# Optimization experiments

Hardware: AMD Instinct MI355X
Metric: run time of the kernel (lower is better)

Reference implementation:

```python
import jax, jax.numpy as jnp
import numpy as np

BATCH = 2048
NUM_SEEN = 32768
HIDDEN = 768
GAMMA_INIT = -2.3


def setup_inputs() -> dict:
    key = jax.random.key(0)
    k_h, k_s, k_v, k_g = jax.random.split(key, 4)
    h = jax.random.normal(k_h, (BATCH, HIDDEN), dtype=jnp.float32)
    # sigmoid gate scores in [0, 1]
    s = jax.random.uniform(k_s, (BATCH, NUM_SEEN), dtype=jnp.float32)
    # unit spurious directions (rows normalized, as in set_directions usage)
    V = jax.random.normal(k_v, (NUM_SEEN, HIDDEN), dtype=jnp.float32)
    V = V / jnp.linalg.norm(V, axis=1, keepdims=True)
    log_gamma = jnp.float32(GAMMA_INIT)
    return {"h": h, "s": s, "V": V, "log_gamma": log_gamma, "top_k": 64}


def top_k_gate(s, k):
    # keep top-k scores per row, zero the rest
    if k <= 0:
        return s
    k = min(k, s.shape[1])
    vals, idx = jax.lax.top_k(s, k)            # [B, k]
    rows = jnp.arange(s.shape[0])[:, None]      # [B, 1]
    return jnp.zeros_like(s).at[rows, idx].set(vals)


def reference(h, s, V, log_gamma, top_k):
    gamma = jax.nn.softplus(log_gamma)
    s_sparse = top_k_gate(s, top_k)
    proj = h @ V.T                              # [B, num_seen]
    raw_signal = (s_sparse * proj) @ V          # [B, hidden]
    return h - gamma * raw_signal
```

## Files before the change

kernel.cpp:

```cpp
#include <hip/hip_runtime.h>
#include <math.h>


constexpr int NSEEN  = 32768;
constexpr int HIDDEN = 768;
constexpr int NBINS  = 2048;
constexpr int SEG    = NBINS / 256;
constexpr int CAP    = 2048;
constexpr int KMAX   = 64;

__device__ inline unsigned int ordkey(float x) {
    unsigned int u = __float_as_uint(x);
    return (u & 0x80000000u) ? ~u : (u | 0x80000000u);
}
__device__ inline float ordkey_inv(unsigned int o) {
    unsigned int u = (o & 0x80000000u) ? (o ^ 0x80000000u) : ~o;
    return __uint_as_float(u);
}

__device__ inline int bucket_of(float x, int mode, float lo, float scale) {
    if (mode == 0) {
        if (x < lo) return -1;
        int b = (int)((x - lo) * scale);
        return (b > NBINS - 1) ? (NBINS - 1) : b;
    } else {
        return (int)(ordkey(x) >> 21);
    }
}

__global__ __launch_bounds__(256)
void stl_topk_kernel(const float* __restrict__ H,
                     const float* __restrict__ S,
                     const float* __restrict__ V,
                     const float* __restrict__ LG,
                     const int*   __restrict__ KP,
                     float* __restrict__ OUT)
{
    const int row  = blockIdx.x;
    const int tid  = threadIdx.x;
    const int lane = tid & 63;
    const int wav  = tid >> 6;

    __shared__ unsigned int hist[NBINS];
    __shared__ unsigned long long cand[CAP];
    __shared__ float hlds[HIDDEN];
    __shared__ unsigned int suff[256];
    __shared__ float coef[KMAX];
    __shared__ float selval[KMAX];
    __shared__ unsigned int selidx[KMAX];
    __shared__ unsigned int scount;
    __shared__ int sbin;
    __shared__ int sseg;

    int k = KP[0];
    if (k < 1)    k = 1;
    if (k > KMAX) k = KMAX;

    const float lgv   = LG[0];
    const float gamma = (lgv > 20.f) ? lgv : log1pf(expf(lgv));

    const float* hrow = H + (size_t)row * HIDDEN;
    for (int c = tid; c < HIDDEN; c += 256) hlds[c] = hrow[c];

    const float4* srow4 = (const float4*)(S + (size_t)row * NSEEN);

    int   mode  = 0;
    float lo    = 0.98f;
    float scale = (float)NBINS / 0.02f;
    int   B     = 0;

    for (int attempt = 0; attempt < 2; ++attempt) {
        for (int b = tid; b < NBINS; b += 256) hist[b] = 0;
        __syncthreads();

        for (int i = tid; i < NSEEN / 4; i += 256) {
            float4 v = srow4[i];
            float xs[4] = {v.x, v.y, v.z, v.w};
            #pragma unroll
            for (int c = 0; c < 4; ++c) {
                int b = bucket_of(xs[c], mode, lo, scale);
                if (b >= 0) atomicAdd(&hist[b], 1u);
            }
        }
        __syncthreads();

        unsigned int ps = 0;
        #pragma unroll
        for (int u = 0; u < SEG; ++u) ps += hist[tid * SEG + u];
        suff[tid] = ps;
        __syncthreads();
        for (int d = 1; d < 256; d <<= 1) {
            unsigned int add = (tid + d < 256) ? suff[tid + d] : 0u;
            __syncthreads();
            suff[tid] += add;
            __syncthreads();
        }

        unsigned int total = suff[0];
        if (total >= (unsigned)k) {
            if (suff[tid] >= (unsigned)k && (tid == 255 || suff[tid + 1] < (unsigned)k))
                sseg = tid;
            __syncthreads();
            if (tid == 0) {
                int t = sseg;
                unsigned int running = (t < 255) ? suff[t + 1] : 0u;
                int b = t * SEG + SEG - 1;
                for (; b > t * SEG; --b) {
                    running += hist[b];
                    if (running >= (unsigned)k) break;
                }
                if (running < (unsigned)k) {  running += hist[b]; }
                sbin   = b;
                scount = 0;
            }
            __syncthreads();
            B = sbin;
            break;
        }
        mode = 1;
        __syncthreads();
    }

    for (int i = tid; i < NSEEN / 4; i += 256) {
        float4 v = srow4[i];
        float xs[4] = {v.x, v.y, v.z, v.w};
        #pragma unroll
        for (int c = 0; c < 4; ++c) {
            float x = xs[c];
            int b = bucket_of(x, mode, lo, scale);
            if (b >= B) {
                unsigned int pos = atomicAdd(&scount, 1u);
                if (pos < CAP) {
                    unsigned int idx = (unsigned int)(4 * i + c);
                    cand[pos] = ((unsigned long long)ordkey(x) << 32) | (unsigned int)(~idx);
                }
            }
        }
    }
    __syncthreads();

    unsigned int C = scount;
    if (C > CAP) C = CAP;

    if (wav == 0) {
        for (int j = 0; j < k; ++j) {
            unsigned long long best = 0ULL;
            int bslot = 0;
            for (int p = lane; p < (int)C; p += 64) {
                unsigned long long key = cand[p];
                if (key > best) { best = key; bslot = p; }
            }
            #pragma unroll
            for (int d = 32; d >= 1; d >>= 1) {
                unsigned long long ok = __shfl_xor(best, d, 64);
                int os = __shfl_xor(bslot, d, 64);
                if (ok > best) { best = ok; bslot = os; }
            }
            if (lane == 0) {
                selval[j] = ordkey_inv((unsigned int)(best >> 32));
                selidx[j] = ~(unsigned int)(best & 0xFFFFFFFFu);
            }
            cand[bslot] = 0ULL;
        }
    }
    __syncthreads();

    for (int j = wav; j < k; j += 4) {
        const float* vrow = V + (size_t)selidx[j] * HIDDEN;
        float p = 0.f;
        #pragma unroll
        for (int t = 0; t < HIDDEN / 64; ++t) {
            int c = lane + 64 * t;
            p += hlds[c] * vrow[c];
        }
        #pragma unroll
        for (int d = 1; d < 64; d <<= 1) p += __shfl_xor(p, d, 64);
        if (lane == 0) coef[j] = selval[j] * p;
    }
    __syncthreads();

    float acc0 = 0.f, acc1 = 0.f, acc2 = 0.f;
    for (int j = 0; j < k; ++j) {
        const float cf = coef[j];
        const float* vrow = V + (size_t)selidx[j] * HIDDEN;
        acc0 += cf * vrow[tid];
        acc1 += cf * vrow[tid + 256];
        acc2 += cf * vrow[tid + 512];
    }
    float* orow = OUT + (size_t)row * HIDDEN;
    orow[tid]       = hlds[tid]       - gamma * acc0;
    orow[tid + 256] = hlds[tid + 256] - gamma * acc1;
    orow[tid + 512] = hlds[tid + 512] - gamma * acc2;
}

extern "C" void kernel_launch(void* const* d_in, const int* in_sizes, int n_in,
                              void* d_out, int out_size, void* d_ws, size_t ws_size,
                              hipStream_t stream) {
    const float* H  = (const float*)d_in[0];
    const float* S  = (const float*)d_in[1];
    const float* V  = (const float*)d_in[2];
    const float* LG = (const float*)d_in[3];
    const int*   KP = (const int*)d_in[4];
    float* OUT = (float*)d_out;

    const int rows = in_sizes[1] / NSEEN;
    stl_topk_kernel<<<dim3(rows), dim3(256), 0, stream>>>(H, S, V, LG, KP, OUT);
}
```

Before: 590.4 us.

## Fuse histogram and candidate gather into one pass with wave-aggregated pushes

Builds the histogram and collects all candidates above the fixed threshold in a single pass over the score row, instead of one histogram pass followed by a second gather pass. Per-element LDS atomics on the counter are replaced with ballot-based wave-aggregated appends. Candidates strictly above the boundary bin are taken directly, so the serial argmax loop only runs over the remaining boundary-bin elements. The dot product is vectorized with float4 loads, and bins and capacity are halved. This adds ballot and shuffle overhead on every element, and the fallback path now needs three row passes when the threshold fails.

```diff
diff --git a/kernel.cpp b/kernel.cpp
--- a/kernel.cpp
+++ b/kernel.cpp
@@ -2,29 +2,43 @@
 #include <math.h>
 
 
-constexpr int NSEEN  = 32768;
-constexpr int HIDDEN = 768;
-constexpr int NBINS  = 2048;
-constexpr int SEG    = NBINS / 256;
-constexpr int CAP    = 2048;
-constexpr int KMAX   = 64;
-
-__device__ inline unsigned int ordkey(float x) {
-    unsigned int u = __float_as_uint(x);
+constexpr int   NSEEN  = 32768;
+constexpr int   HIDDEN = 768;
+constexpr int   NBINS  = 1024;
+constexpr int   SEG    = NBINS / 256;
+constexpr int   CAP    = 1024;
+constexpr int   KMAX   = 64;
+constexpr float LO     = 0.98f;
+
+__device__ inline unsigned ordkey(float x) {
+    unsigned u = __float_as_uint(x);
     return (u & 0x80000000u) ? ~u : (u | 0x80000000u);
 }
-__device__ inline float ordkey_inv(unsigned int o) {
-    unsigned int u = (o & 0x80000000u) ? (o ^ 0x80000000u) : ~o;
+__device__ inline float ordkey_inv(unsigned o) {
+    unsigned u = (o & 0x80000000u) ? (o ^ 0x80000000u) : ~o;
     return __uint_as_float(u);
 }
-
-__device__ inline int bucket_of(float x, int mode, float lo, float scale) {
+__device__ inline int bucket_of(float x, int mode, float scale) {
     if (mode == 0) {
-        if (x < lo) return -1;
-        int b = (int)((x - lo) * scale);
+        if (x < LO) return -1;
+        int b = (int)((x - LO) * scale);
         return (b > NBINS - 1) ? (NBINS - 1) : b;
-    } else {
-        return (int)(ordkey(x) >> 21);
+    }
+    return (int)(ordkey(x) >> 22);
+}
+
+__device__ inline void wave_push(bool pred, unsigned long long key, int lane,
+                                 unsigned* counter, unsigned long long* buf, int cap) {
+    unsigned long long m = __ballot(pred);
+    if (m) {
+        int leader = __ffsll((unsigned long long)m) - 1;
+        unsigned base = 0;
+        if (lane == leader) base = atomicAdd(counter, (unsigned)__popcll(m));
+        base = __shfl(base, leader, 64);
+        if (pred) {
+            unsigned pos = base + (unsigned)__popcll(m & ((1ULL << lane) - 1ULL));
+            if (pos < (unsigned)cap) buf[pos] = key;
+        }
     }
 }
 
@@ -41,16 +55,17 @@
     const int lane = tid & 63;
     const int wav  = tid >> 6;
 
-    __shared__ unsigned int hist[NBINS];
+    __shared__ unsigned hist[NBINS];
     __shared__ unsigned long long cand[CAP];
-    __shared__ float hlds[HIDDEN];
-    __shared__ unsigned int suff[256];
+    __shared__ __align__(16) float hlds[HIDDEN];
+    __shared__ unsigned suff[256];
+    __shared__ unsigned long long selkey[KMAX];
+    __shared__ float selval[KMAX];
+    __shared__ unsigned selidx[KMAX];
     __shared__ float coef[KMAX];
-    __shared__ float selval[KMAX];
-    __shared__ unsigned int selidx[KMAX];
-    __shared__ unsigned int scount;
-    __shared__ int sbin;
-    __shared__ int sseg;
+    __shared__ unsigned scount, ssel;
+    __shared__ int sseg, sbin;
+    __shared__ unsigned scnt_gt;
 
     int k = KP[0];
     if (k < 1)    k = 1;
@@ -58,97 +73,126 @@
 
     const float lgv   = LG[0];
     const float gamma = (lgv > 20.f) ? lgv : log1pf(expf(lgv));
+    const float scale = (float)NBINS / (1.0f - LO);
 
     const float* hrow = H + (size_t)row * HIDDEN;
     for (int c = tid; c < HIDDEN; c += 256) hlds[c] = hrow[c];
 
     const float4* srow4 = (const float4*)(S + (size_t)row * NSEEN);
 
-    int   mode  = 0;
-    float lo    = 0.98f;
-    float scale = (float)NBINS / 0.02f;
-    int   B     = 0;
-
-    for (int attempt = 0; attempt < 2; ++attempt) {
-        for (int b = tid; b < NBINS; b += 256) hist[b] = 0;
-        __syncthreads();
-
-        for (int i = tid; i < NSEEN / 4; i += 256) {
-            float4 v = srow4[i];
-            float xs[4] = {v.x, v.y, v.z, v.w};
-            #pragma unroll
-            for (int c = 0; c < 4; ++c) {
-                int b = bucket_of(xs[c], mode, lo, scale);
-                if (b >= 0) atomicAdd(&hist[b], 1u);
-            }
-        }
-        __syncthreads();
-
-        unsigned int ps = 0;
-        #pragma unroll
-        for (int u = 0; u < SEG; ++u) ps += hist[tid * SEG + u];
-        suff[tid] = ps;
-        __syncthreads();
-        for (int d = 1; d < 256; d <<= 1) {
-            unsigned int add = (tid + d < 256) ? suff[tid + d] : 0u;
-            __syncthreads();
-            suff[tid] += add;
-            __syncthreads();
-        }
-
-        unsigned int total = suff[0];
-        if (total >= (unsigned)k) {
-            if (suff[tid] >= (unsigned)k && (tid == 255 || suff[tid + 1] < (unsigned)k))
-                sseg = tid;
-            __syncthreads();
-            if (tid == 0) {
-                int t = sseg;
-                unsigned int running = (t < 255) ? suff[t + 1] : 0u;
-                int b = t * SEG + SEG - 1;
-                for (; b > t * SEG; --b) {
-                    running += hist[b];
-                    if (running >= (unsigned)k) break;
-                }
-                if (running < (unsigned)k) {  running += hist[b]; }
-                sbin   = b;
-                scount = 0;
-            }
-            __syncthreads();
-            B = sbin;
-            break;
-        }
-        mode = 1;
-        __syncthreads();
-    }
-
+    for (int b = tid; b < NBINS; b += 256) hist[b] = 0;
+    if (tid == 0) scount = 0;
+    __syncthreads();
+
+    int mode = 0;
     for (int i = tid; i < NSEEN / 4; i += 256) {
         float4 v = srow4[i];
         float xs[4] = {v.x, v.y, v.z, v.w};
         #pragma unroll
         for (int c = 0; c < 4; ++c) {
             float x = xs[c];
-            int b = bucket_of(x, mode, lo, scale);
-            if (b >= B) {
-                unsigned int pos = atomicAdd(&scount, 1u);
-                if (pos < CAP) {
-                    unsigned int idx = (unsigned int)(4 * i + c);
-                    cand[pos] = ((unsigned long long)ordkey(x) << 32) | (unsigned int)(~idx);
-                }
-            }
-        }
-    }
-    __syncthreads();
-
-    unsigned int C = scount;
-    if (C > CAP) C = CAP;
+            bool pred = (x >= LO);
+            if (pred) {
+                int b = bucket_of(x, 0, scale);
+                atomicAdd(&hist[b], 1u);
+            }
+            unsigned idx = (unsigned)(4 * i + c);
+            unsigned long long key =
+                ((unsigned long long)ordkey(x) << 32) | (unsigned)(~idx);
+            wave_push(pred, key, lane, &scount, cand, CAP);
+        }
+    }
+    __syncthreads();
+
+    unsigned C = scount;
+
+    if (C < (unsigned)k || C > (unsigned)CAP) {
+        mode = 1;
+        for (int b = tid; b < NBINS; b += 256) hist[b] = 0;
+        __syncthreads();
+        for (int i = tid; i < NSEEN / 4; i += 256) {
+            float4 v = srow4[i];
+            float xs[4] = {v.x, v.y, v.z, v.w};
+            #pragma unroll
+            for (int c = 0; c < 4; ++c)
+                atomicAdd(&hist[bucket_of(xs[c], 1, scale)], 1u);
+        }
+        __syncthreads();
+    }
+
+    unsigned ps = 0;
+    #pragma unroll
+    for (int u = 0; u < SEG; ++u) ps += hist[tid * SEG + u];
+    suff[tid] = ps;
+    __syncthreads();
+    for (int d = 1; d < 256; d <<= 1) {
+        unsigned add = (tid + d < 256) ? suff[tid + d] : 0u;
+        __syncthreads();
+        suff[tid] += add;
+        __syncthreads();
+    }
+    if (suff[tid] >= (unsigned)k && (tid == 255 || suff[tid + 1] < (unsigned)k))
+        sseg = tid;
+    __syncthreads();
+    if (tid == 0) {
+        int t = sseg;
+        unsigned running = (t < 255) ? suff[t + 1] : 0u;
+        int b = t * SEG + SEG - 1;
+        for (;;) {
+            running += hist[b];
+            if (running >= (unsigned)k || b == t * SEG) break;
+            --b;
+        }
+        sbin    = b;
+        scnt_gt = running - hist[b];
+        ssel    = 0;
+    }
+    __syncthreads();
+
+    const int B = sbin;
+    const unsigned cnt_gt = scnt_gt;
+
+    if (mode == 1) {
+        if (tid == 0) scount = 0;
+        __syncthreads();
+        for (int i = tid; i < NSEEN / 4; i += 256) {
+            float4 v = srow4[i];
+            float xs[4] = {v.x, v.y, v.z, v.w};
+            #pragma unroll
+            for (int c = 0; c < 4; ++c) {
+                float x = xs[c];
+                bool pred = (bucket_of(x, 1, scale) >= B);
+                unsigned idx = (unsigned)(4 * i + c);
+                unsigned long long key =
+                    ((unsigned long long)ordkey(x) << 32) | (unsigned)(~idx);
+                wave_push(pred, key, lane, &scount, cand, CAP);
+            }
+        }
+        __syncthreads();
+        C = scount < (unsigned)CAP ? scount : (unsigned)CAP;
+    }
+
+    for (int p = tid; p < (int)C; p += 256) {
+        unsigned long long key = cand[p];
+        float val = ordkey_inv((unsigned)(key >> 32));
+        bool pred = (bucket_of(val, mode, scale) > B);
+        wave_push(pred, key, lane, &ssel, selkey, KMAX);
+    }
+    __syncthreads();
 
     if (wav == 0) {
-        for (int j = 0; j < k; ++j) {
+        const int r = k - (int)cnt_gt;
+        for (int it = 0; it < r; ++it) {
             unsigned long long best = 0ULL;
-            int bslot = 0;
+            int bslot = -1;
             for (int p = lane; p < (int)C; p += 64) {
                 unsigned long long key = cand[p];
-                if (key > best) { best = key; bslot = p; }
+                if (key) {
+                    float val = ordkey_inv((unsigned)(key >> 32));
+                    if (bucket_of(val, mode, scale) == B && key > best) {
+                        best = key; bslot = p;
+                    }
+                }
             }
             #pragma unroll
             for (int d = 32; d >= 1; d >>= 1) {
@@ -157,21 +201,29 @@
                 if (ok > best) { best = ok; bslot = os; }
             }
             if (lane == 0) {
-                selval[j] = ordkey_inv((unsigned int)(best >> 32));
-                selidx[j] = ~(unsigned int)(best & 0xFFFFFFFFu);
-            }
-            cand[bslot] = 0ULL;
-        }
-    }
-    __syncthreads();
-
+                selkey[cnt_gt + it] = best;
+                cand[bslot] = 0ULL;
+            }
+        }
+    }
+    __syncthreads();
+
+    if (tid < k) {
+        unsigned long long key = selkey[tid];
+        selval[tid] = ordkey_inv((unsigned)(key >> 32));
+        selidx[tid] = ~(unsigned)(key & 0xFFFFFFFFu);
+    }
+    __syncthreads();
+
+    const float4* hl4 = (const float4*)hlds;
     for (int j = wav; j < k; j += 4) {
-        const float* vrow = V + (size_t)selidx[j] * HIDDEN;
+        const float4* vr4 = (const float4*)(V + (size_t)selidx[j] * HIDDEN);
         float p = 0.f;
         #pragma unroll
-        for (int t = 0; t < HIDDEN / 64; ++t) {
-            int c = lane + 64 * t;
-            p += hlds[c] * vrow[c];
+        for (int t = 0; t < HIDDEN / 256; ++t) {
+            float4 a  = vr4[lane + 64 * t];
+            float4 hq = hl4[lane + 64 * t];
+            p += a.x * hq.x + a.y * hq.y + a.z * hq.z + a.w * hq.w;
         }
         #pragma unroll
         for (int d = 1; d < 64; d <<= 1) p += __shfl_xor(p, d, 64);
```

Result: faster. 511.9 us (-13.3%).
